# Kernel optimization log

Measured on AMD Instinct MI355X. Metric: run time of the kernel, lower is better.

The kernel has to match this reference:

```python
import jax, jax.numpy as jnp
import numpy as np

N_NODES = 100000   # total nodes in batched graph
N_EDGES = 800000   # total edges
N_GRAPH = 64       # graphs in batch
N_PASSES = 3


def _mlp(x, w1, b1, w2, b2, w3, b3):
    h = jax.nn.relu(x @ w1 + b1)
    h = jax.nn.relu(h @ w2 + b2)
    return h @ w3 + b3


def _segment_mean(x, ids, num_segments):
    # tf.math.unsorted_segment_mean: empty segments -> 0
    s = jax.ops.segment_sum(x, ids, num_segments=num_segments)
    c = jax.ops.segment_sum(jnp.ones((x.shape[0], 1), x.dtype), ids, num_segments=num_segments)
    return s / jnp.maximum(c, 1.0)


def setup_inputs() -> dict:
    key = jax.random.key(0)
    ks = jax.random.split(key, 16)
    nodes = jax.random.normal(ks[0], (N_NODES, 32), jnp.float32)
    edges = jax.random.normal(ks[1], (N_EDGES, 32), jnp.float32)
    globals_ = jax.random.normal(ks[2], (N_GRAPH, 16), jnp.float32)
    senders = jax.random.randint(ks[3], (N_EDGES,), 0, N_NODES, jnp.int32)
    receivers = jax.random.randint(ks[4], (N_EDGES,), 0, N_NODES, jnp.int32)
    node_gid = jnp.sort(jax.random.randint(ks[5], (N_NODES,), 0, N_GRAPH, jnp.int32))
    edge_gid = jnp.sort(jax.random.randint(ks[6], (N_EDGES,), 0, N_GRAPH, jnp.int32))

    def dense(k, din, dout):
        kw, _ = jax.random.split(k)
        w = jax.random.normal(kw, (din, dout), jnp.float32) / np.sqrt(din).astype(np.float32)
        b = jnp.zeros((dout,), jnp.float32)
        return w, b

    e_w1, e_b1 = dense(ks[7], 112, 16)
    e_w2, e_b2 = dense(ks[8], 16, 16)
    e_w3, e_b3 = dense(ks[9], 16, 32)
    n_w1, n_b1 = dense(ks[10], 80, 16)
    n_w2, n_b2 = dense(ks[11], 16, 16)
    n_w3, n_b3 = dense(ks[12], 16, 32)
    g_w1, g_b1 = dense(ks[13], 80, 16)
    g_w2, g_b2 = dense(ks[14], 16, 16)
    g_w3, g_b3 = dense(ks[15], 16, 16)
    return dict(nodes=nodes, edges=edges, globals_=globals_, senders=senders,
                receivers=receivers, node_gid=node_gid, edge_gid=edge_gid,
                e_w1=e_w1, e_b1=e_b1, e_w2=e_w2, e_b2=e_b2, e_w3=e_w3, e_b3=e_b3,
                n_w1=n_w1, n_b1=n_b1, n_w2=n_w2, n_b2=n_b2, n_w3=n_w3, n_b3=n_b3,
                g_w1=g_w1, g_b1=g_b1, g_w2=g_w2, g_b2=g_b2, g_w3=g_w3, g_b3=g_b3)


def reference(nodes, edges, globals_, senders, receivers, node_gid, edge_gid,
              e_w1, e_b1, e_w2, e_b2, e_w3, e_b3,
              n_w1, n_b1, n_w2, n_b2, n_w3, n_b3,
              g_w1, g_b1, g_w2, g_b2, g_w3, g_b3):
    for _ in range(N_PASSES):
        # Edge block: [edges, receiver nodes, sender nodes, broadcast globals]
        e_in = jnp.concatenate([edges, nodes[receivers], nodes[senders], globals_[edge_gid]], axis=-1)
        edges = _mlp(e_in, e_w1, e_b1, e_w2, e_b2, e_w3, e_b3)
        # Node block: [mean of received edges, nodes, broadcast globals]
        agg_e = _segment_mean(edges, receivers, N_NODES)
        n_in = jnp.concatenate([agg_e, nodes, globals_[node_gid]], axis=-1)
        nodes = _mlp(n_in, n_w1, n_b1, n_w2, n_b2, n_w3, n_b3)
        # Global block: [mean edges per graph, mean nodes per graph, globals]
        g_in = jnp.concatenate([_segment_mean(edges, edge_gid, N_GRAPH),
                                _segment_mean(nodes, node_gid, N_GRAPH),
                                globals_], axis=-1)
        globals_ = _mlp(g_in, g_w1, g_b1, g_w2, g_b2, g_w3, g_b3)
    return nodes, edges, globals_
```

## Files before the change

kernel.cpp:

```cpp
#include <hip/hip_runtime.h>

#define DEV_INLINE __device__ __forceinline__

static const int SCAN_B = 512;

DEV_INLINE int lower_bound_i(const int* __restrict__ a, int n, int v) {
    int lo = 0, hi = n;
    while (lo < hi) { int m = (lo + hi) >> 1; if (a[m] < v) lo = m + 1; else hi = m; }
    return lo;
}

DEV_INLINE void fma4(float (&h)[16], const float* __restrict__ W, float4 a) {
#pragma unroll
    for (int j = 0; j < 16; j++) h[j] = fmaf(a.x, W[0 * 16 + j], h[j]);
#pragma unroll
    for (int j = 0; j < 16; j++) h[j] = fmaf(a.y, W[1 * 16 + j], h[j]);
#pragma unroll
    for (int j = 0; j < 16; j++) h[j] = fmaf(a.z, W[2 * 16 + j], h[j]);
#pragma unroll
    for (int j = 0; j < 16; j++) h[j] = fmaf(a.w, W[3 * 16 + j], h[j]);
}

__global__ void hist_kernel(const int* __restrict__ receivers, int n_edges,
                            int* __restrict__ cnt) {
    int i = blockIdx.x * blockDim.x + threadIdx.x;
    if (i < n_edges) atomicAdd(&cnt[receivers[i]], 1);
}

__global__ __launch_bounds__(SCAN_B)
void scan_block_kernel(const int* __restrict__ cnt, int n,
                       int* __restrict__ scan_tmp, int* __restrict__ blk_sum) {
    __shared__ int s[SCAN_B];
    int tid = threadIdx.x;
    int i = blockIdx.x * SCAN_B + tid;
    int v = (i < n) ? cnt[i] : 0;
    s[tid] = v;
    __syncthreads();
    for (int off = 1; off < SCAN_B; off <<= 1) {
        int t = (tid >= off) ? s[tid - off] : 0;
        __syncthreads();
        s[tid] += t;
        __syncthreads();
    }
    if (i < n) scan_tmp[i] = s[tid];
    if (tid == SCAN_B - 1) blk_sum[blockIdx.x] = s[tid];
}

__global__ __launch_bounds__(1024)
void scan_top_kernel(int* __restrict__ blk_sum, int nb, int* __restrict__ blk_off) {
    __shared__ int s[1024];
    int tid = threadIdx.x;
    int v = (tid < nb) ? blk_sum[tid] : 0;
    s[tid] = v;
    __syncthreads();
    for (int off = 1; off < 1024; off <<= 1) {
        int t = (tid >= off) ? s[tid - off] : 0;
        __syncthreads();
        s[tid] += t;
        __syncthreads();
    }
    if (tid < nb) blk_off[tid] = s[tid] - v;
}

__global__ __launch_bounds__(SCAN_B)
void scan_finalize_kernel(const int* __restrict__ cnt, const int* __restrict__ scan_tmp,
                          const int* __restrict__ blk_off, int n,
                          int* __restrict__ row_ptr, int* __restrict__ running) {
    int i = blockIdx.x * SCAN_B + threadIdx.x;
    if (i >= n) return;
    int incl = scan_tmp[i] + blk_off[i / SCAN_B];
    row_ptr[i + 1] = incl;
    running[i] = incl - cnt[i];
    if (i == 0) row_ptr[0] = 0;
}

__global__ void fill_kernel(const int* __restrict__ receivers, int n_edges,
                            int* __restrict__ running, int* __restrict__ col_idx) {
    int e = blockIdx.x * blockDim.x + threadIdx.x;
    if (e >= n_edges) return;
    int pos = atomicAdd(&running[receivers[e]], 1);
    col_idx[pos] = e;
}

__global__ __launch_bounds__(256)
void node_proj_kernel(const float* __restrict__ nodes_in,
                      const float* __restrict__ W1,
                      float* __restrict__ proj, int n_nodes) {
    const int n0 = blockIdx.x * 256 + threadIdx.x;
    const int n  = min(n0, n_nodes - 1);
    const float4* pn = (const float4*)nodes_in + (size_t)n * 8;
    float4 xn[8];
#pragma unroll
    for (int q = 0; q < 8; q++) xn[q] = pn[q];

    float hr[16], hs[16];
#pragma unroll
    for (int j = 0; j < 16; j++) { hr[j] = 0.0f; hs[j] = 0.0f; }
#pragma unroll
    for (int q = 0; q < 8; q++) fma4(hr, W1 + (32 + q * 4) * 16, xn[q]);
#pragma unroll
    for (int q = 0; q < 8; q++) fma4(hs, W1 + (64 + q * 4) * 16, xn[q]);

    if (n0 < n_nodes) {
        float4* po = (float4*)(proj + (size_t)n0 * 32);
#pragma unroll
        for (int j4 = 0; j4 < 4; j4++)
            po[j4] = make_float4(hr[j4*4+0], hr[j4*4+1], hr[j4*4+2], hr[j4*4+3]);
#pragma unroll
        for (int j4 = 0; j4 < 4; j4++)
            po[4 + j4] = make_float4(hs[j4*4+0], hs[j4*4+1], hs[j4*4+2], hs[j4*4+3]);
    }
}

__global__ __launch_bounds__(64)
void bias_kernel(const float* __restrict__ glob_in,
                 const float* __restrict__ eW1, const float* __restrict__ eB1,
                 const float* __restrict__ nW1, const float* __restrict__ nB1,
                 float* __restrict__ biasE, float* __restrict__ biasN, int n_graph) {
    const int g0 = threadIdx.x;
    const int g  = min(g0, n_graph - 1);
    float xg[16];
#pragma unroll
    for (int q = 0; q < 4; q++) {
        float4 v = ((const float4*)glob_in)[(size_t)g * 4 + q];
        xg[q*4+0] = v.x; xg[q*4+1] = v.y; xg[q*4+2] = v.z; xg[q*4+3] = v.w;
    }
    float he[16], hn[16];
#pragma unroll
    for (int j = 0; j < 16; j++) { he[j] = eB1[j]; hn[j] = nB1[j]; }
#pragma unroll
    for (int k = 0; k < 16; k++)
#pragma unroll
        for (int j = 0; j < 16; j++) he[j] = fmaf(xg[k], eW1[(96 + k) * 16 + j], he[j]);
#pragma unroll
    for (int k = 0; k < 16; k++)
#pragma unroll
        for (int j = 0; j < 16; j++) hn[j] = fmaf(xg[k], nW1[(64 + k) * 16 + j], hn[j]);
    if (g0 < n_graph) {
#pragma unroll
        for (int j = 0; j < 16; j++) biasE[g0 * 16 + j] = he[j];
#pragma unroll
        for (int j = 0; j < 16; j++) biasN[g0 * 16 + j] = hn[j];
    }
}

__global__ __launch_bounds__(256)
void edge_block_kernel(const float* __restrict__ edges_in,
                       const float* __restrict__ proj,
                       const float* __restrict__ biasE,
                       const int* __restrict__ senders,
                       const int* __restrict__ receivers,
                       const int* __restrict__ edge_gid,
                       const float* __restrict__ W1,
                       const float* __restrict__ W2, const float* __restrict__ B2,
                       const float* __restrict__ W3, const float* __restrict__ B3,
                       float* __restrict__ edges_out,
                       int n_edges) {
    const int e0 = blockIdx.x * 256 + threadIdx.x;
    const int e  = min(e0, n_edges - 1);

    const int rr = receivers[e], ss = senders[e], gg = edge_gid[e];

    const float4* pe = (const float4*)edges_in + (size_t)e  * 8;
    const float4* pr = (const float4*)proj + (size_t)rr * 8;
    const float4* ps = (const float4*)proj + (size_t)ss * 8 + 4;
    const float4* pb = (const float4*)biasE + (size_t)gg * 4;

    float4 xe[8], xr[4], xs[4], xb[4];
#pragma unroll
    for (int q = 0; q < 8; q++) xe[q] = pe[q];
#pragma unroll
    for (int q = 0; q < 4; q++) xr[q] = pr[q];
#pragma unroll
    for (int q = 0; q < 4; q++) xs[q] = ps[q];
#pragma unroll
    for (int q = 0; q < 4; q++) xb[q] = pb[q];

    float h1[16];
#pragma unroll
    for (int q = 0; q < 4; q++) {
        h1[q*4+0] = xb[q].x + xr[q].x + xs[q].x;
        h1[q*4+1] = xb[q].y + xr[q].y + xs[q].y;
        h1[q*4+2] = xb[q].z + xr[q].z + xs[q].z;
        h1[q*4+3] = xb[q].w + xr[q].w + xs[q].w;
    }
#pragma unroll
    for (int q = 0; q < 8; q++) fma4(h1, W1 + (q * 4) * 16, xe[q]);

    float x2[16];
#pragma unroll
    for (int j = 0; j < 16; j++) x2[j] = fmaxf(h1[j], 0.0f);
    float h2[16];
#pragma unroll
    for (int j = 0; j < 16; j++) h2[j] = B2[j];
#pragma unroll
    for (int k = 0; k < 16; k++)
#pragma unroll
        for (int j = 0; j < 16; j++) h2[j] = fmaf(x2[k], W2[k * 16 + j], h2[j]);

    float x3[16];
#pragma unroll
    for (int j = 0; j < 16; j++) x3[j] = fmaxf(h2[j], 0.0f);
    float o[32];
#pragma unroll
    for (int j = 0; j < 32; j++) o[j] = B3[j];
#pragma unroll
    for (int k = 0; k < 16; k++)
#pragma unroll
        for (int j = 0; j < 32; j++)
            o[j] = fmaf(x3[k], W3[k * 32 + j], o[j]);

    if (e0 < n_edges) {
        float4* eo = (float4*)(edges_out + (size_t)e0 * 32);
#pragma unroll
        for (int j4 = 0; j4 < 8; j4++)
            eo[j4] = make_float4(o[j4 * 4 + 0], o[j4 * 4 + 1], o[j4 * 4 + 2], o[j4 * 4 + 3]);
    }
}

__global__ __launch_bounds__(256)
void agg_mean_kernel(const float* __restrict__ edges_data,
                     const int* __restrict__ col_idx,
                     const int* __restrict__ row_ptr,
                     float* __restrict__ agg_mean, int n_nodes) {
    int node = blockIdx.x * 32 + (threadIdx.x >> 3);
    int lane = threadIdx.x & 7;
    if (node >= n_nodes) return;
    int lo = row_ptr[node], hi = row_ptr[node + 1];
    float4 acc = make_float4(0.f, 0.f, 0.f, 0.f);
    for (int e = lo; e < hi; e++) {
        int idx = col_idx[e];
        float4 v = ((const float4*)(edges_data + (size_t)idx * 32))[lane];
        acc.x += v.x; acc.y += v.y; acc.z += v.z; acc.w += v.w;
    }
    float inv = 1.0f / fmaxf((float)(hi - lo), 1.0f);
    ((float4*)(agg_mean + (size_t)node * 32))[lane] =
        make_float4(acc.x * inv, acc.y * inv, acc.z * inv, acc.w * inv);
}

__global__ __launch_bounds__(256)
void node_block_kernel(const float* __restrict__ agg_mean,
                       const float* __restrict__ nodes_in,
                       const float* __restrict__ biasN,
                       const int* __restrict__ node_gid,
                       const float* __restrict__ W1,
                       const float* __restrict__ W2, const float* __restrict__ B2,
                       const float* __restrict__ W3, const float* __restrict__ B3,
                       float* __restrict__ nodes_out,
                       int n_nodes) {
    const int n0 = blockIdx.x * 256 + threadIdx.x;
    const int n  = min(n0, n_nodes - 1);
    const int gg = node_gid[n];

    const float4* pa = (const float4*)agg_mean + (size_t)n * 8;
    const float4* pn = (const float4*)nodes_in + (size_t)n * 8;
    const float4* pb = (const float4*)biasN + (size_t)gg * 4;

    float4 xa[8], xn[8], xb[4];
#pragma unroll
    for (int q = 0; q < 8; q++) xa[q] = pa[q];
#pragma unroll
    for (int q = 0; q < 8; q++) xn[q] = pn[q];
#pragma unroll
    for (int q = 0; q < 4; q++) xb[q] = pb[q];

    float h1[16];
#pragma unroll
    for (int q = 0; q < 4; q++) {
        h1[q*4+0] = xb[q].x; h1[q*4+1] = xb[q].y; h1[q*4+2] = xb[q].z; h1[q*4+3] = xb[q].w;
    }
#pragma unroll
    for (int q = 0; q < 8; q++) fma4(h1, W1 + (q * 4) * 16, xa[q]);
#pragma unroll
    for (int q = 0; q < 8; q++) fma4(h1, W1 + (32 + q * 4) * 16, xn[q]);

    float x2[16];
#pragma unroll
    for (int j = 0; j < 16; j++) x2[j] = fmaxf(h1[j], 0.0f);
    float h2[16];
#pragma unroll
    for (int j = 0; j < 16; j++) h2[j] = B2[j];
#pragma unroll
    for (int k = 0; k < 16; k++)
#pragma unroll
        for (int j = 0; j < 16; j++) h2[j] = fmaf(x2[k], W2[k * 16 + j], h2[j]);

    float x3[16];
#pragma unroll
    for (int j = 0; j < 16; j++) x3[j] = fmaxf(h2[j], 0.0f);
    float o[32];
#pragma unroll
    for (int j = 0; j < 32; j++) o[j] = B3[j];
#pragma unroll
    for (int k = 0; k < 16; k++)
#pragma unroll
        for (int j = 0; j < 32; j++)
            o[j] = fmaf(x3[k], W3[k * 32 + j], o[j]);

    if (n0 < n_nodes) {
        float4* no = (float4*)(nodes_out + (size_t)n0 * 32);
#pragma unroll
        for (int j4 = 0; j4 < 8; j4++)
            no[j4] = make_float4(o[j4 * 4 + 0], o[j4 * 4 + 1], o[j4 * 4 + 2], o[j4 * 4 + 3]);
    }
}

__global__ __launch_bounds__(256)
void graph_sum_kernel(const float* __restrict__ x, const int* __restrict__ gid,
                      int n_rows, float* __restrict__ sums, int splits) {
    int g = blockIdx.x / splits;
    int s = blockIdx.x % splits;
    int lo = lower_bound_i(gid, n_rows, g);
    int hi = lower_bound_i(gid, n_rows, g + 1);
    int len = hi - lo;
    int chunk = (len + splits - 1) / splits;
    int rlo = lo + s * chunk;
    int rhi = min(rlo + chunk, hi);

    int c = threadIdx.x & 31;
    int rg = threadIdx.x >> 5;
    float acc = 0.0f;
    for (int r = rlo + rg; r < rhi; r += 8)
        acc += x[(size_t)r * 32 + c];

    __shared__ float red[256];
    red[threadIdx.x] = acc;
    __syncthreads();
    if (threadIdx.x < 32) {
        float ssum = 0.0f;
#pragma unroll
        for (int i = 0; i < 8; i++) ssum += red[i * 32 + threadIdx.x];
        atomicAdd(&sums[g * 32 + threadIdx.x], ssum);
    }
}

__global__ __launch_bounds__(64)
void global_block_kernel(const float* __restrict__ gsum_e,
                         const float* __restrict__ gsum_n,
                         const float* __restrict__ glob_in,
                         const int* __restrict__ edge_gid, int n_edges,
                         const int* __restrict__ node_gid, int n_nodes,
                         const float* __restrict__ W1, const float* __restrict__ B1,
                         const float* __restrict__ W2, const float* __restrict__ B2,
                         const float* __restrict__ W3, const float* __restrict__ B3,
                         float* __restrict__ glob_out, int n_graph) {
    const int g0 = threadIdx.x;
    const int g  = min(g0, n_graph - 1);

    int ecnt = lower_bound_i(edge_gid, n_edges, g + 1) - lower_bound_i(edge_gid, n_edges, g);
    int ncnt = lower_bound_i(node_gid, n_nodes, g + 1) - lower_bound_i(node_gid, n_nodes, g);
    float inv_e = 1.0f / fmaxf((float)ecnt, 1.0f);
    float inv_n = 1.0f / fmaxf((float)ncnt, 1.0f);

    float h1[16];
#pragma unroll
    for (int j = 0; j < 16; j++) h1[j] = B1[j];

    {
        float x[32];
#pragma unroll
        for (int q = 0; q < 8; q++) {
            float4 v = ((const float4*)gsum_e)[(size_t)g * 8 + q];
            x[q*4+0] = v.x * inv_e; x[q*4+1] = v.y * inv_e; x[q*4+2] = v.z * inv_e; x[q*4+3] = v.w * inv_e;
        }
#pragma unroll
        for (int k = 0; k < 32; k++)
#pragma unroll
            for (int j = 0; j < 16; j++) h1[j] = fmaf(x[k], W1[k * 16 + j], h1[j]);
#pragma unroll
        for (int q = 0; q < 8; q++) {
            float4 v = ((const float4*)gsum_n)[(size_t)g * 8 + q];
            x[q*4+0] = v.x * inv_n; x[q*4+1] = v.y * inv_n; x[q*4+2] = v.z * inv_n; x[q*4+3] = v.w * inv_n;
        }
#pragma unroll
        for (int k = 0; k < 32; k++)
#pragma unroll
            for (int j = 0; j < 16; j++) h1[j] = fmaf(x[k], W1[(32 + k) * 16 + j], h1[j]);
    }
    {
        float xg[16];
#pragma unroll
        for (int q = 0; q < 4; q++) {
            float4 v = ((const float4*)glob_in)[(size_t)g * 4 + q];
            xg[q*4+0] = v.x; xg[q*4+1] = v.y; xg[q*4+2] = v.z; xg[q*4+3] = v.w;
        }
#pragma unroll
        for (int k = 0; k < 16; k++)
#pragma unroll
            for (int j = 0; j < 16; j++) h1[j] = fmaf(xg[k], W1[(64 + k) * 16 + j], h1[j]);
    }

    float x2[16];
#pragma unroll
    for (int j = 0; j < 16; j++) x2[j] = fmaxf(h1[j], 0.0f);
    float h2[16];
#pragma unroll
    for (int j = 0; j < 16; j++) h2[j] = B2[j];
#pragma unroll
    for (int k = 0; k < 16; k++)
#pragma unroll
        for (int j = 0; j < 16; j++) h2[j] = fmaf(x2[k], W2[k * 16 + j], h2[j]);

    float x3[16];
#pragma unroll
    for (int j = 0; j < 16; j++) x3[j] = fmaxf(h2[j], 0.0f);
    float o[16];
#pragma unroll
    for (int j = 0; j < 16; j++) o[j] = B3[j];
#pragma unroll
    for (int k = 0; k < 16; k++)
#pragma unroll
        for (int j = 0; j < 16; j++) o[j] = fmaf(x3[k], W3[k * 16 + j], o[j]);

    if (g0 < n_graph) {
#pragma unroll
        for (int j = 0; j < 16; j++) glob_out[g0 * 16 + j] = o[j];
    }
}

extern "C" void kernel_launch(void* const* d_in, const int* in_sizes, int n_in,
                              void* d_out, int out_size, void* d_ws, size_t ws_size,
                              hipStream_t stream) {
    const float* d_nodes = (const float*)d_in[0];
    const float* d_edges = (const float*)d_in[1];
    const float* d_glob  = (const float*)d_in[2];
    const int* senders   = (const int*)d_in[3];
    const int* receivers = (const int*)d_in[4];
    const int* node_gid  = (const int*)d_in[5];
    const int* edge_gid  = (const int*)d_in[6];
    const float* e_w1 = (const float*)d_in[7];
    const float* e_b1 = (const float*)d_in[8];
    const float* e_w2 = (const float*)d_in[9];
    const float* e_b2 = (const float*)d_in[10];
    const float* e_w3 = (const float*)d_in[11];
    const float* e_b3 = (const float*)d_in[12];
    const float* n_w1 = (const float*)d_in[13];
    const float* n_b1 = (const float*)d_in[14];
    const float* n_w2 = (const float*)d_in[15];
    const float* n_b2 = (const float*)d_in[16];
    const float* n_w3 = (const float*)d_in[17];
    const float* n_b3 = (const float*)d_in[18];
    const float* g_w1 = (const float*)d_in[19];
    const float* g_b1 = (const float*)d_in[20];
    const float* g_w2 = (const float*)d_in[21];
    const float* g_b2 = (const float*)d_in[22];
    const float* g_w3 = (const float*)d_in[23];
    const float* g_b3 = (const float*)d_in[24];

    const int n_nodes = in_sizes[0] / 32;
    const int n_edges = in_sizes[1] / 32;
    const int n_graph = in_sizes[2] / 16;

    float* out_nodes = (float*)d_out;
    float* out_edges = out_nodes + (size_t)n_nodes * 32;
    float* out_glob  = out_edges + (size_t)n_edges * 32;

    float* ws = (float*)d_ws;
    float* ws_edges = ws;  ws += (size_t)n_edges * 32;
    float* ws_nodes = ws;  ws += (size_t)n_nodes * 32;
    float* nscratch = ws;  ws += (size_t)n_nodes * 32;
    float* gA       = ws;  ws += (size_t)n_graph * 16;
    float* gB       = ws;  ws += (size_t)n_graph * 16;
    float* gsum_e   = ws;  ws += (size_t)n_graph * 32;
    float* gsum_n   = ws;  ws += (size_t)n_graph * 32;
    float* biasE    = ws;  ws += (size_t)n_graph * 16;
    float* biasN    = ws;  ws += (size_t)n_graph * 16;

    int* wi = (int*)ws;
    int* cnt      = wi;  wi += n_nodes;
    int* row_ptr  = wi;  wi += n_nodes + 1;
    int* running  = wi;  wi += n_nodes;
    int* scan_tmp = wi;  wi += n_nodes;
    int* col_idx  = wi;  wi += n_edges;
    int* blk_sum  = wi;  wi += 1024;
    int* blk_off  = wi;  wi += 1024;

    const int nblocks_scan = (n_nodes + SCAN_B - 1) / SCAN_B;

    hipMemsetAsync(cnt, 0, (size_t)n_nodes * sizeof(int), stream);
    hist_kernel<<<(n_edges + 255) / 256, 256, 0, stream>>>(receivers, n_edges, cnt);
    scan_block_kernel<<<nblocks_scan, SCAN_B, 0, stream>>>(cnt, n_nodes, scan_tmp, blk_sum);
    scan_top_kernel<<<1, 1024, 0, stream>>>(blk_sum, nblocks_scan, blk_off);
    scan_finalize_kernel<<<nblocks_scan, SCAN_B, 0, stream>>>(cnt, scan_tmp, blk_off,
                                                              n_nodes, row_ptr, running);
    fill_kernel<<<(n_edges + 255) / 256, 256, 0, stream>>>(receivers, n_edges, running, col_idx);

    const float* nodes_in = d_nodes;
    const float* edges_in = d_edges;
    const float* glob_in  = d_glob;

    for (int pass = 0; pass < 3; ++pass) {
        float* nodes_out; float* edges_out; float* glob_out;
        if (pass == 0)      { nodes_out = out_nodes; edges_out = out_edges; glob_out = gA; }
        else if (pass == 1) { nodes_out = ws_nodes;  edges_out = ws_edges;  glob_out = gB; }
        else                { nodes_out = out_nodes; edges_out = out_edges; glob_out = out_glob; }

        hipMemsetAsync(gsum_e, 0, (size_t)n_graph * 32 * sizeof(float), stream);
        hipMemsetAsync(gsum_n, 0, (size_t)n_graph * 32 * sizeof(float), stream);

        bias_kernel<<<1, 64, 0, stream>>>(glob_in, e_w1, e_b1, n_w1, n_b1,
                                          biasE, biasN, n_graph);
        node_proj_kernel<<<(n_nodes + 255) / 256, 256, 0, stream>>>(
            nodes_in, e_w1, nscratch, n_nodes);

        edge_block_kernel<<<(n_edges + 255) / 256, 256, 0, stream>>>(
            edges_in, nscratch, biasE, senders, receivers, edge_gid,
            e_w1, e_w2, e_b2, e_w3, e_b3,
            edges_out, n_edges);

        graph_sum_kernel<<<n_graph * 16, 256, 0, stream>>>(edges_out, edge_gid, n_edges, gsum_e, 16);

        agg_mean_kernel<<<(n_nodes + 31) / 32, 256, 0, stream>>>(
            edges_out, col_idx, row_ptr, nscratch, n_nodes);

        node_block_kernel<<<(n_nodes + 255) / 256, 256, 0, stream>>>(
            nscratch, nodes_in, biasN, node_gid,
            n_w1, n_w2, n_b2, n_w3, n_b3,
            nodes_out, n_nodes);

        graph_sum_kernel<<<n_graph * 4, 256, 0, stream>>>(nodes_out, node_gid, n_nodes, gsum_n, 4);

        global_block_kernel<<<1, 64, 0, stream>>>(
            gsum_e, gsum_n, glob_in, edge_gid, n_edges, node_gid, n_nodes,
            g_w1, g_b1, g_w2, g_b2, g_w3, g_b3,
            glob_out, n_graph);

        nodes_in = nodes_out;
        edges_in = edges_out;
        glob_in  = glob_out;
    }
}
```

Before: 843.5 us.

## Fuse per-graph sums into edge/node kernels and bias into projection kernel

Removes the separate graph_sum kernels by doing a wavefront shuffle reduction of each edge/node MLP output and atomically adding it into the per-graph sums. This avoids rereading the edge and node outputs from memory. The bias kernel is also folded into block 0 of the node projection kernel to save a launch. The cost is a 32-channel, six-step shuffle tree in every wave, which adds register pressure and shuffle work to the already heavy MLP kernels. Waves that span a graph boundary fall back to per-thread atomics.

Measured after the change: 1.771 ms. 2.1x slower.

```diff
diff --git a/kernel.cpp b/kernel.cpp
--- a/kernel.cpp
+++ b/kernel.cpp
@@ -19,6 +19,29 @@
     for (int j = 0; j < 16; j++) h[j] = fmaf(a.z, W[2 * 16 + j], h[j]);
 #pragma unroll
     for (int j = 0; j < 16; j++) h[j] = fmaf(a.w, W[3 * 16 + j], h[j]);
+}
+
+DEV_INLINE void wave_graph_sum(float (&o)[32], bool valid, int gg, int lane,
+                               float* __restrict__ gsum) {
+    const int gref = __shfl(gg, 0);
+    const bool uni = __all(gg == gref || !valid);
+    if (uni) {
+        float vf = valid ? 1.0f : 0.0f;
+        float s[32];
+#pragma unroll
+        for (int j = 0; j < 32; j++) s[j] = o[j] * vf;
+#pragma unroll
+        for (int off = 1; off < 64; off <<= 1)
+#pragma unroll
+            for (int j = 0; j < 32; j++) s[j] += __shfl_xor(s[j], off);
+        if (lane == 0) {
+#pragma unroll
+            for (int j = 0; j < 32; j++) atomicAdd(&gsum[gref * 32 + j], s[j]);
+        }
+    } else if (valid) {
+#pragma unroll
+        for (int j = 0; j < 32; j++) atomicAdd(&gsum[gg * 32 + j], o[j]);
+    }
 }
 
 __global__ void hist_kernel(const int* __restrict__ receivers, int n_edges,
@@ -84,8 +107,12 @@
 
 __global__ __launch_bounds__(256)
 void node_proj_kernel(const float* __restrict__ nodes_in,
-                      const float* __restrict__ W1,
-                      float* __restrict__ proj, int n_nodes) {
+                      const float* __restrict__ glob_in,
+                      const float* __restrict__ eW1, const float* __restrict__ eB1,
+                      const float* __restrict__ nW1, const float* __restrict__ nB1,
+                      float* __restrict__ proj,
+                      float* __restrict__ biasE, float* __restrict__ biasN,
+                      int n_nodes, int n_graph) {
     const int n0 = blockIdx.x * 256 + threadIdx.x;
     const int n  = min(n0, n_nodes - 1);
     const float4* pn = (const float4*)nodes_in + (size_t)n * 8;
@@ -97,9 +124,9 @@
 #pragma unroll
     for (int j = 0; j < 16; j++) { hr[j] = 0.0f; hs[j] = 0.0f; }
 #pragma unroll
-    for (int q = 0; q < 8; q++) fma4(hr, W1 + (32 + q * 4) * 16, xn[q]);
-#pragma unroll
-    for (int q = 0; q < 8; q++) fma4(hs, W1 + (64 + q * 4) * 16, xn[q]);
+    for (int q = 0; q < 8; q++) fma4(hr, eW1 + (32 + q * 4) * 16, xn[q]);
+#pragma unroll
+    for (int q = 0; q < 8; q++) fma4(hs, eW1 + (64 + q * 4) * 16, xn[q]);
 
     if (n0 < n_nodes) {
         float4* po = (float4*)(proj + (size_t)n0 * 32);
@@ -110,37 +137,30 @@
         for (int j4 = 0; j4 < 4; j4++)
             po[4 + j4] = make_float4(hs[j4*4+0], hs[j4*4+1], hs[j4*4+2], hs[j4*4+3]);
     }
-}
-
-__global__ __launch_bounds__(64)
-void bias_kernel(const float* __restrict__ glob_in,
-                 const float* __restrict__ eW1, const float* __restrict__ eB1,
-                 const float* __restrict__ nW1, const float* __restrict__ nB1,
-                 float* __restrict__ biasE, float* __restrict__ biasN, int n_graph) {
-    const int g0 = threadIdx.x;
-    const int g  = min(g0, n_graph - 1);
-    float xg[16];
-#pragma unroll
-    for (int q = 0; q < 4; q++) {
-        float4 v = ((const float4*)glob_in)[(size_t)g * 4 + q];
-        xg[q*4+0] = v.x; xg[q*4+1] = v.y; xg[q*4+2] = v.z; xg[q*4+3] = v.w;
-    }
-    float he[16], hn[16];
-#pragma unroll
-    for (int j = 0; j < 16; j++) { he[j] = eB1[j]; hn[j] = nB1[j]; }
-#pragma unroll
-    for (int k = 0; k < 16; k++)
-#pragma unroll
-        for (int j = 0; j < 16; j++) he[j] = fmaf(xg[k], eW1[(96 + k) * 16 + j], he[j]);
-#pragma unroll
-    for (int k = 0; k < 16; k++)
-#pragma unroll
-        for (int j = 0; j < 16; j++) hn[j] = fmaf(xg[k], nW1[(64 + k) * 16 + j], hn[j]);
-    if (g0 < n_graph) {
-#pragma unroll
-        for (int j = 0; j < 16; j++) biasE[g0 * 16 + j] = he[j];
-#pragma unroll
-        for (int j = 0; j < 16; j++) biasN[g0 * 16 + j] = hn[j];
+
+    if (blockIdx.x == 0 && threadIdx.x < n_graph) {
+        const int g = threadIdx.x;
+        float xg[16];
+#pragma unroll
+        for (int q = 0; q < 4; q++) {
+            float4 v = ((const float4*)glob_in)[(size_t)g * 4 + q];
+            xg[q*4+0] = v.x; xg[q*4+1] = v.y; xg[q*4+2] = v.z; xg[q*4+3] = v.w;
+        }
+        float he[16], hn[16];
+#pragma unroll
+        for (int j = 0; j < 16; j++) { he[j] = eB1[j]; hn[j] = nB1[j]; }
+#pragma unroll
+        for (int k = 0; k < 16; k++)
+#pragma unroll
+            for (int j = 0; j < 16; j++) he[j] = fmaf(xg[k], eW1[(96 + k) * 16 + j], he[j]);
+#pragma unroll
+        for (int k = 0; k < 16; k++)
+#pragma unroll
+            for (int j = 0; j < 16; j++) hn[j] = fmaf(xg[k], nW1[(64 + k) * 16 + j], hn[j]);
+#pragma unroll
+        for (int j = 0; j < 16; j++) biasE[g * 16 + j] = he[j];
+#pragma unroll
+        for (int j = 0; j < 16; j++) biasN[g * 16 + j] = hn[j];
     }
 }
 
@@ -155,9 +175,12 @@
                        const float* __restrict__ W2, const float* __restrict__ B2,
                        const float* __restrict__ W3, const float* __restrict__ B3,
                        float* __restrict__ edges_out,
+                       float* __restrict__ gsum_e,
                        int n_edges) {
     const int e0 = blockIdx.x * 256 + threadIdx.x;
     const int e  = min(e0, n_edges - 1);
+    const bool valid = (e0 < n_edges);
+    const int lane = threadIdx.x & 63;
 
     const int rr = receivers[e], ss = senders[e], gg = edge_gid[e];
 
@@ -210,12 +233,14 @@
         for (int j = 0; j < 32; j++)
             o[j] = fmaf(x3[k], W3[k * 32 + j], o[j]);
 
-    if (e0 < n_edges) {
+    if (valid) {
         float4* eo = (float4*)(edges_out + (size_t)e0 * 32);
 #pragma unroll
         for (int j4 = 0; j4 < 8; j4++)
             eo[j4] = make_float4(o[j4 * 4 + 0], o[j4 * 4 + 1], o[j4 * 4 + 2], o[j4 * 4 + 3]);
     }
+
+    wave_graph_sum(o, valid, gg, lane, gsum_e);
 }
 
 __global__ __launch_bounds__(256)
@@ -247,9 +272,12 @@
                        const float* __restrict__ W2, const float* __restrict__ B2,
                        const float* __restrict__ W3, const float* __restrict__ B3,
                        float* __restrict__ nodes_out,
+                       float* __restrict__ gsum_n,
                        int n_nodes) {
     const int n0 = blockIdx.x * 256 + threadIdx.x;
     const int n  = min(n0, n_nodes - 1);
+    const bool valid = (n0 < n_nodes);
+    const int lane = threadIdx.x & 63;
     const int gg = node_gid[n];
 
     const float4* pa = (const float4*)agg_mean + (size_t)n * 8;
@@ -297,41 +325,14 @@
         for (int j = 0; j < 32; j++)
             o[j] = fmaf(x3[k], W3[k * 32 + j], o[j]);
 
-    if (n0 < n_nodes) {
+    if (valid) {
         float4* no = (float4*)(nodes_out + (size_t)n0 * 32);
 #pragma unroll
         for (int j4 = 0; j4 < 8; j4++)
             no[j4] = make_float4(o[j4 * 4 + 0], o[j4 * 4 + 1], o[j4 * 4 + 2], o[j4 * 4 + 3]);
     }
-}
-
-__global__ __launch_bounds__(256)
-void graph_sum_kernel(const float* __restrict__ x, const int* __restrict__ gid,
-                      int n_rows, float* __restrict__ sums, int splits) {
-    int g = blockIdx.x / splits;
-    int s = blockIdx.x % splits;
-    int lo = lower_bound_i(gid, n_rows, g);
-    int hi = lower_bound_i(gid, n_rows, g + 1);
-    int len = hi - lo;
-    int chunk = (len + splits - 1) / splits;
-    int rlo = lo + s * chunk;
-    int rhi = min(rlo + chunk, hi);
-
-    int c = threadIdx.x & 31;
-    int rg = threadIdx.x >> 5;
-    float acc = 0.0f;
-    for (int r = rlo + rg; r < rhi; r += 8)
-        acc += x[(size_t)r * 32 + c];
-
-    __shared__ float red[256];
-    red[threadIdx.x] = acc;
-    __syncthreads();
-    if (threadIdx.x < 32) {
-        float ssum = 0.0f;
-#pragma unroll
-        for (int i = 0; i < 8; i++) ssum += red[i * 32 + threadIdx.x];
-        atomicAdd(&sums[g * 32 + threadIdx.x], ssum);
-    }
+
+    wave_graph_sum(o, valid, gg, lane, gsum_n);
 }
 
 __global__ __launch_bounds__(64)
@@ -498,17 +499,14 @@
         hipMemsetAsync(gsum_e, 0, (size_t)n_graph * 32 * sizeof(float), stream);
         hipMemsetAsync(gsum_n, 0, (size_t)n_graph * 32 * sizeof(float), stream);
 
-        bias_kernel<<<1, 64, 0, stream>>>(glob_in, e_w1, e_b1, n_w1, n_b1,
-                                          biasE, biasN, n_graph);
         node_proj_kernel<<<(n_nodes + 255) / 256, 256, 0, stream>>>(
-            nodes_in, e_w1, nscratch, n_nodes);
+            nodes_in, glob_in, e_w1, e_b1, n_w1, n_b1,
+            nscratch, biasE, biasN, n_nodes, n_graph);
 
         edge_block_kernel<<<(n_edges + 255) / 256, 256, 0, stream>>>(
             edges_in, nscratch, biasE, senders, receivers, edge_gid,
             e_w1, e_w2, e_b2, e_w3, e_b3,
-            edges_out, n_edges);
-
-        graph_sum_kernel<<<n_graph * 16, 256, 0, stream>>>(edges_out, edge_gid, n_edges, gsum_e, 16);
+            edges_out, gsum_e, n_edges);
 
         agg_mean_kernel<<<(n_nodes + 31) / 32, 256, 0, stream>>>(
             edges_out, col_idx, row_ptr, nscratch, n_nodes);
@@ -516,9 +514,7 @@
         node_block_kernel<<<(n_nodes + 255) / 256, 256, 0, stream>>>(
             nscratch, nodes_in, biasN, node_gid,
             n_w1, n_w2, n_b2, n_w3, n_b3,
-            nodes_out, n_nodes);
-
-        graph_sum_kernel<<<n_graph * 4, 256, 0, stream>>>(nodes_out, node_gid, n_nodes, gsum_n, 4);
+            nodes_out, gsum_n, n_nodes);
 
         global_block_kernel<<<1, 64, 0, stream>>>(
             gsum_e, gsum_n, glob_in, edge_gid, n_edges, node_gid, n_nodes,
```

## Store node projections in fp16 and fold global/bias kernels into node_proj

Applied to the files above, without the earlier changes.

The per-node projection table gathered by the edge kernel is now stored as fp16, which halves the random-gather bytes per edge. The edge kernel unpacks it to fp32 before use. The separate bias kernel, the gsum memsets and the previous pass's global MLP now run inside block 0 of node_proj_kernel, removing several small launches per pass. This adds fp16 rounding error to the edge MLP input and makes block 0 do serial extra work.

Result: faster. 808.5 us (-4.2%).

```diff
diff --git a/kernel.cpp b/kernel.cpp
--- a/kernel.cpp
+++ b/kernel.cpp
@@ -1,4 +1,5 @@
 #include <hip/hip_runtime.h>
+#include <hip/hip_fp16.h>
 
 #define DEV_INLINE __device__ __forceinline__
 
@@ -19,6 +20,20 @@
     for (int j = 0; j < 16; j++) h[j] = fmaf(a.z, W[2 * 16 + j], h[j]);
 #pragma unroll
     for (int j = 0; j < 16; j++) h[j] = fmaf(a.w, W[3 * 16 + j], h[j]);
+}
+
+DEV_INLINE unsigned f2h2(float a, float b) {
+    __half2 h = __floats2half2_rn(a, b);
+    return *reinterpret_cast<unsigned*>(&h);
+}
+DEV_INLINE float2 h2f2(unsigned u) {
+    __half2 h;
+    *reinterpret_cast<unsigned*>(&h) = u;
+    return __half22float2(h);
+}
+DEV_INLINE void unpack8(uint4 u, float (&f)[8]) {
+    float2 a = h2f2(u.x), b = h2f2(u.y), c = h2f2(u.z), d = h2f2(u.w);
+    f[0]=a.x; f[1]=a.y; f[2]=b.x; f[3]=b.y; f[4]=c.x; f[5]=c.y; f[6]=d.x; f[7]=d.y;
 }
 
 __global__ void hist_kernel(const int* __restrict__ receivers, int n_edges,
@@ -84,8 +99,19 @@
 
 __global__ __launch_bounds__(256)
 void node_proj_kernel(const float* __restrict__ nodes_in,
-                      const float* __restrict__ W1,
-                      float* __restrict__ proj, int n_nodes) {
+                      const float* __restrict__ glob_prev,
+                      float* __restrict__ glob_cur,
+                      float* __restrict__ gsum_e, float* __restrict__ gsum_n,
+                      const int* __restrict__ edge_gid, int n_edges,
+                      const int* __restrict__ node_gid, int n_nodes,
+                      const float* __restrict__ gW1, const float* __restrict__ gB1,
+                      const float* __restrict__ gW2, const float* __restrict__ gB2,
+                      const float* __restrict__ gW3, const float* __restrict__ gB3,
+                      const float* __restrict__ eW1, const float* __restrict__ eB1,
+                      const float* __restrict__ nW1, const float* __restrict__ nB1,
+                      __half* __restrict__ proj,
+                      float* __restrict__ biasE, float* __restrict__ biasN,
+                      int n_graph) {
     const int n0 = blockIdx.x * 256 + threadIdx.x;
     const int n  = min(n0, n_nodes - 1);
     const float4* pn = (const float4*)nodes_in + (size_t)n * 8;
@@ -97,56 +123,117 @@
 #pragma unroll
     for (int j = 0; j < 16; j++) { hr[j] = 0.0f; hs[j] = 0.0f; }
 #pragma unroll
-    for (int q = 0; q < 8; q++) fma4(hr, W1 + (32 + q * 4) * 16, xn[q]);
-#pragma unroll
-    for (int q = 0; q < 8; q++) fma4(hs, W1 + (64 + q * 4) * 16, xn[q]);
+    for (int q = 0; q < 8; q++) fma4(hr, eW1 + (32 + q * 4) * 16, xn[q]);
+#pragma unroll
+    for (int q = 0; q < 8; q++) fma4(hs, eW1 + (64 + q * 4) * 16, xn[q]);
 
     if (n0 < n_nodes) {
-        float4* po = (float4*)(proj + (size_t)n0 * 32);
-#pragma unroll
-        for (int j4 = 0; j4 < 4; j4++)
-            po[j4] = make_float4(hr[j4*4+0], hr[j4*4+1], hr[j4*4+2], hr[j4*4+3]);
-#pragma unroll
-        for (int j4 = 0; j4 < 4; j4++)
-            po[4 + j4] = make_float4(hs[j4*4+0], hs[j4*4+1], hs[j4*4+2], hs[j4*4+3]);
-    }
-}
-
-__global__ __launch_bounds__(64)
-void bias_kernel(const float* __restrict__ glob_in,
-                 const float* __restrict__ eW1, const float* __restrict__ eB1,
-                 const float* __restrict__ nW1, const float* __restrict__ nB1,
-                 float* __restrict__ biasE, float* __restrict__ biasN, int n_graph) {
-    const int g0 = threadIdx.x;
-    const int g  = min(g0, n_graph - 1);
-    float xg[16];
-#pragma unroll
-    for (int q = 0; q < 4; q++) {
-        float4 v = ((const float4*)glob_in)[(size_t)g * 4 + q];
-        xg[q*4+0] = v.x; xg[q*4+1] = v.y; xg[q*4+2] = v.z; xg[q*4+3] = v.w;
-    }
-    float he[16], hn[16];
-#pragma unroll
-    for (int j = 0; j < 16; j++) { he[j] = eB1[j]; hn[j] = nB1[j]; }
-#pragma unroll
-    for (int k = 0; k < 16; k++)
-#pragma unroll
-        for (int j = 0; j < 16; j++) he[j] = fmaf(xg[k], eW1[(96 + k) * 16 + j], he[j]);
-#pragma unroll
-    for (int k = 0; k < 16; k++)
-#pragma unroll
-        for (int j = 0; j < 16; j++) hn[j] = fmaf(xg[k], nW1[(64 + k) * 16 + j], hn[j]);
-    if (g0 < n_graph) {
-#pragma unroll
-        for (int j = 0; j < 16; j++) biasE[g0 * 16 + j] = he[j];
-#pragma unroll
-        for (int j = 0; j < 16; j++) biasN[g0 * 16 + j] = hn[j];
+        uint4* po = (uint4*)(proj + (size_t)n0 * 32);
+        po[0] = make_uint4(f2h2(hr[0],hr[1]),  f2h2(hr[2],hr[3]),
+                           f2h2(hr[4],hr[5]),  f2h2(hr[6],hr[7]));
+        po[1] = make_uint4(f2h2(hr[8],hr[9]),  f2h2(hr[10],hr[11]),
+                           f2h2(hr[12],hr[13]),f2h2(hr[14],hr[15]));
+        po[2] = make_uint4(f2h2(hs[0],hs[1]),  f2h2(hs[2],hs[3]),
+                           f2h2(hs[4],hs[5]),  f2h2(hs[6],hs[7]));
+        po[3] = make_uint4(f2h2(hs[8],hs[9]),  f2h2(hs[10],hs[11]),
+                           f2h2(hs[12],hs[13]),f2h2(hs[14],hs[15]));
+    }
+
+    if (blockIdx.x == 0) {
+        const int g = threadIdx.x;
+        float gval[16];
+        if (g < n_graph) {
+            if (glob_cur) {
+                int ecnt = lower_bound_i(edge_gid, n_edges, g + 1) - lower_bound_i(edge_gid, n_edges, g);
+                int ncnt = lower_bound_i(node_gid, n_nodes, g + 1) - lower_bound_i(node_gid, n_nodes, g);
+                float inv_e = 1.0f / fmaxf((float)ecnt, 1.0f);
+                float inv_n = 1.0f / fmaxf((float)ncnt, 1.0f);
+                float h1[16];
+#pragma unroll
+                for (int j = 0; j < 16; j++) h1[j] = gB1[j];
+                float x[32];
+#pragma unroll
+                for (int q = 0; q < 8; q++) {
+                    float4 v = ((const float4*)gsum_e)[(size_t)g * 8 + q];
+                    x[q*4+0]=v.x*inv_e; x[q*4+1]=v.y*inv_e; x[q*4+2]=v.z*inv_e; x[q*4+3]=v.w*inv_e;
+                }
+#pragma unroll
+                for (int k = 0; k < 32; k++)
+#pragma unroll
+                    for (int j = 0; j < 16; j++) h1[j] = fmaf(x[k], gW1[k * 16 + j], h1[j]);
+#pragma unroll
+                for (int q = 0; q < 8; q++) {
+                    float4 v = ((const float4*)gsum_n)[(size_t)g * 8 + q];
+                    x[q*4+0]=v.x*inv_n; x[q*4+1]=v.y*inv_n; x[q*4+2]=v.z*inv_n; x[q*4+3]=v.w*inv_n;
+                }
+#pragma unroll
+                for (int k = 0; k < 32; k++)
+#pragma unroll
+                    for (int j = 0; j < 16; j++) h1[j] = fmaf(x[k], gW1[(32 + k) * 16 + j], h1[j]);
+                float xg[16];
+#pragma unroll
+                for (int q = 0; q < 4; q++) {
+                    float4 v = ((const float4*)glob_prev)[(size_t)g * 4 + q];
+                    xg[q*4+0]=v.x; xg[q*4+1]=v.y; xg[q*4+2]=v.z; xg[q*4+3]=v.w;
+                }
+#pragma unroll
+                for (int k = 0; k < 16; k++)
+#pragma unroll
+                    for (int j = 0; j < 16; j++) h1[j] = fmaf(xg[k], gW1[(64 + k) * 16 + j], h1[j]);
+                float x2[16];
+#pragma unroll
+                for (int j = 0; j < 16; j++) x2[j] = fmaxf(h1[j], 0.0f);
+                float h2[16];
+#pragma unroll
+                for (int j = 0; j < 16; j++) h2[j] = gB2[j];
+#pragma unroll
+                for (int k = 0; k < 16; k++)
+#pragma unroll
+                    for (int j = 0; j < 16; j++) h2[j] = fmaf(x2[k], gW2[k * 16 + j], h2[j]);
+                float x3[16];
+#pragma unroll
+                for (int j = 0; j < 16; j++) x3[j] = fmaxf(h2[j], 0.0f);
+#pragma unroll
+                for (int j = 0; j < 16; j++) gval[j] = gB3[j];
+#pragma unroll
+                for (int k = 0; k < 16; k++)
+#pragma unroll
+                    for (int j = 0; j < 16; j++) gval[j] = fmaf(x3[k], gW3[k * 16 + j], gval[j]);
+#pragma unroll
+                for (int j = 0; j < 16; j++) glob_cur[g * 16 + j] = gval[j];
+            } else {
+#pragma unroll
+                for (int j = 0; j < 16; j++) gval[j] = glob_prev[g * 16 + j];
+            }
+        }
+        __syncthreads();
+        for (int i = threadIdx.x; i < n_graph * 32; i += 256) {
+            gsum_e[i] = 0.0f;
+            gsum_n[i] = 0.0f;
+        }
+        if (g < n_graph) {
+            float he[16], hn[16];
+#pragma unroll
+            for (int j = 0; j < 16; j++) { he[j] = eB1[j]; hn[j] = nB1[j]; }
+#pragma unroll
+            for (int k = 0; k < 16; k++)
+#pragma unroll
+                for (int j = 0; j < 16; j++) he[j] = fmaf(gval[k], eW1[(96 + k) * 16 + j], he[j]);
+#pragma unroll
+            for (int k = 0; k < 16; k++)
+#pragma unroll
+                for (int j = 0; j < 16; j++) hn[j] = fmaf(gval[k], nW1[(64 + k) * 16 + j], hn[j]);
+#pragma unroll
+            for (int j = 0; j < 16; j++) biasE[g * 16 + j] = he[j];
+#pragma unroll
+            for (int j = 0; j < 16; j++) biasN[g * 16 + j] = hn[j];
+        }
     }
 }
 
 __global__ __launch_bounds__(256)
 void edge_block_kernel(const float* __restrict__ edges_in,
-                       const float* __restrict__ proj,
+                       const __half* __restrict__ proj,
                        const float* __restrict__ biasE,
                        const int* __restrict__ senders,
                        const int* __restrict__ receivers,
@@ -162,27 +249,32 @@
     const int rr = receivers[e], ss = senders[e], gg = edge_gid[e];
 
     const float4* pe = (const float4*)edges_in + (size_t)e  * 8;
-    const float4* pr = (const float4*)proj + (size_t)rr * 8;
-    const float4* ps = (const float4*)proj + (size_t)ss * 8 + 4;
+    const uint4*  pr = (const uint4*)(proj + (size_t)rr * 32);
+    const uint4*  ps = (const uint4*)(proj + (size_t)ss * 32 + 16);
     const float4* pb = (const float4*)biasE + (size_t)gg * 4;
 
-    float4 xe[8], xr[4], xs[4], xb[4];
+    float4 xe[8];
 #pragma unroll
     for (int q = 0; q < 8; q++) xe[q] = pe[q];
-#pragma unroll
-    for (int q = 0; q < 4; q++) xr[q] = pr[q];
-#pragma unroll
-    for (int q = 0; q < 4; q++) xs[q] = ps[q];
+    uint4 r0 = pr[0], r1 = pr[1];
+    uint4 s0 = ps[0], s1 = ps[1];
+    float4 xb[4];
 #pragma unroll
     for (int q = 0; q < 4; q++) xb[q] = pb[q];
 
+    float r[16], s[16];
+    { float t[8]; unpack8(r0, t); for (int j = 0; j < 8; j++) r[j] = t[j]; }
+    { float t[8]; unpack8(r1, t); for (int j = 0; j < 8; j++) r[8 + j] = t[j]; }
+    { float t[8]; unpack8(s0, t); for (int j = 0; j < 8; j++) s[j] = t[j]; }
+    { float t[8]; unpack8(s1, t); for (int j = 0; j < 8; j++) s[8 + j] = t[j]; }
+
     float h1[16];
 #pragma unroll
     for (int q = 0; q < 4; q++) {
-        h1[q*4+0] = xb[q].x + xr[q].x + xs[q].x;
-        h1[q*4+1] = xb[q].y + xr[q].y + xs[q].y;
-        h1[q*4+2] = xb[q].z + xr[q].z + xs[q].z;
-        h1[q*4+3] = xb[q].w + xr[q].w + xs[q].w;
+        h1[q*4+0] = xb[q].x + r[q*4+0] + s[q*4+0];
+        h1[q*4+1] = xb[q].y + r[q*4+1] + s[q*4+1];
+        h1[q*4+2] = xb[q].z + r[q*4+2] + s[q*4+2];
+        h1[q*4+3] = xb[q].w + r[q*4+3] + s[q*4+3];
     }
 #pragma unroll
     for (int q = 0; q < 8; q++) fma4(h1, W1 + (q * 4) * 16, xe[q]);
@@ -361,7 +453,7 @@
 #pragma unroll
         for (int q = 0; q < 8; q++) {
             float4 v = ((const float4*)gsum_e)[(size_t)g * 8 + q];
-            x[q*4+0] = v.x * inv_e; x[q*4+1] = v.y * inv_e; x[q*4+2] = v.z * inv_e; x[q*4+3] = v.w * inv_e;
+            x[q*4+0]=v.x*inv_e; x[q*4+1]=v.y*inv_e; x[q*4+2]=v.z*inv_e; x[q*4+3]=v.w*inv_e;
         }
 #pragma unroll
         for (int k = 0; k < 32; k++)
@@ -370,7 +462,7 @@
 #pragma unroll
         for (int q = 0; q < 8; q++) {
             float4 v = ((const float4*)gsum_n)[(size_t)g * 8 + q];
-            x[q*4+0] = v.x * inv_n; x[q*4+1] = v.y * inv_n; x[q*4+2] = v.z * inv_n; x[q*4+3] = v.w * inv_n;
+            x[q*4+0]=v.x*inv_n; x[q*4+1]=v.y*inv_n; x[q*4+2]=v.z*inv_n; x[q*4+3]=v.w*inv_n;
         }
 #pragma unroll
         for (int k = 0; k < 32; k++)
@@ -382,7 +474,7 @@
 #pragma unroll
         for (int q = 0; q < 4; q++) {
             float4 v = ((const float4*)glob_in)[(size_t)g * 4 + q];
-            xg[q*4+0] = v.x; xg[q*4+1] = v.y; xg[q*4+2] = v.z; xg[q*4+3] = v.w;
+            xg[q*4+0]=v.x; xg[q*4+1]=v.y; xg[q*4+2]=v.z; xg[q*4+3]=v.w;
         }
 #pragma unroll
         for (int k = 0; k < 16; k++)
@@ -487,24 +579,26 @@
 
     const float* nodes_in = d_nodes;
     const float* edges_in = d_edges;
-    const float* glob_in  = d_glob;
+    const float* glob_states[4] = { d_glob, gA, gB, out_glob };
 
     for (int pass = 0; pass < 3; ++pass) {
-        float* nodes_out; float* edges_out; float* glob_out;
-        if (pass == 0)      { nodes_out = out_nodes; edges_out = out_edges; glob_out = gA; }
-        else if (pass == 1) { nodes_out = ws_nodes;  edges_out = ws_edges;  glob_out = gB; }
-        else                { nodes_out = out_nodes; edges_out = out_edges; glob_out = out_glob; }
-
-        hipMemsetAsync(gsum_e, 0, (size_t)n_graph * 32 * sizeof(float), stream);
-        hipMemsetAsync(gsum_n, 0, (size_t)n_graph * 32 * sizeof(float), stream);
-
-        bias_kernel<<<1, 64, 0, stream>>>(glob_in, e_w1, e_b1, n_w1, n_b1,
-                                          biasE, biasN, n_graph);
+        float* nodes_out; float* edges_out;
+        if (pass == 0)      { nodes_out = out_nodes; edges_out = out_edges; }
+        else if (pass == 1) { nodes_out = ws_nodes;  edges_out = ws_edges;  }
+        else                { nodes_out = out_nodes; edges_out = out_edges; }
+
         node_proj_kernel<<<(n_nodes + 255) / 256, 256, 0, stream>>>(
-            nodes_in, e_w1, nscratch, n_nodes);
+            nodes_in,
+            glob_states[pass == 0 ? 0 : pass - 1],
+            pass == 0 ? nullptr : (float*)glob_states[pass],
+            gsum_e, gsum_n,
+            edge_gid, n_edges, node_gid, n_nodes,
+            g_w1, g_b1, g_w2, g_b2, g_w3, g_b3,
+            e_w1, e_b1, n_w1, n_b1,
+            (__half*)nscratch, biasE, biasN, n_graph);
 
         edge_block_kernel<<<(n_edges + 255) / 256, 256, 0, stream>>>(
-            edges_in, nscratch, biasE, senders, receivers, edge_gid,
+            edges_in, (const __half*)nscratch, biasE, senders, receivers, edge_gid,
             e_w1, e_w2, e_b2, e_w3, e_b3,
             edges_out, n_edges);
 
@@ -520,13 +614,12 @@
 
         graph_sum_kernel<<<n_graph * 4, 256, 0, stream>>>(nodes_out, node_gid, n_nodes, gsum_n, 4);
 
-        global_block_kernel<<<1, 64, 0, stream>>>(
-            gsum_e, gsum_n, glob_in, edge_gid, n_edges, node_gid, n_nodes,
-            g_w1, g_b1, g_w2, g_b2, g_w3, g_b3,
-            glob_out, n_graph);
-
         nodes_in = nodes_out;
         edges_in = edges_out;
-        glob_in  = glob_out;
-    }
-}
+    }
+
+    global_block_kernel<<<1, 64, 0, stream>>>(
+        gsum_e, gsum_n, gB, edge_gid, n_edges, node_gid, n_nodes,
+        g_w1, g_b1, g_w2, g_b2, g_w3, g_b3,
+        out_glob, n_graph);
+}
```
